# Kernel optimization log

Hardware: AMD Instinct MI355X
Metric: run time of the kernel (lower is better)

## Reference

```python
import jax, jax.numpy as jnp
import numpy as np

B, T, D, C = 4, 8192, 1024, 64  # batch, seq_len, d_model, chunk_size


def setup_inputs() -> dict:
    key = jax.random.key(0)
    k1, k2, k3 = jax.random.split(key, 3)
    out = jax.random.normal(k1, (B, T, D), jnp.float32)
    W_write = jax.random.normal(k2, (D, D), jnp.float32) / np.float32(np.sqrt(D))
    W_read = jax.random.normal(k3, (D, D), jnp.float32) / np.float32(np.sqrt(D))
    decay = jnp.float32(4.6)                     # torch init: tensor(4.6)
    log_alpha = jnp.log(jnp.float32(0.03))       # torch init: log(memory_alpha)
    return {"out": out, "W_write": W_write, "W_read": W_read,
            "decay": decay, "log_alpha": log_alpha}


def reference(out, W_write, W_read, decay, log_alpha):
    Bd, Td, Dd = out.shape
    nC = Td // C  # T chosen divisible by chunk_size
    out32 = out.astype(jnp.float32)
    gamma = jax.nn.sigmoid(decay)
    log_gamma = jnp.log(gamma)

    v = out32 @ W_write.T                               # proj_write
    wk = jnp.pad(out32[:, :-1], ((0, 0), (1, 0), (0, 0)))  # shift right by 1
    rk = out32

    p = jnp.arange(C)
    diffs = jnp.maximum(p[:, None] - 1 - p[None, :], 0)
    causal = (p[:, None] > p[None, :]).astype(jnp.float32)
    M = jnp.exp(diffs * log_gamma) * causal             # (C, C) intra-chunk decay mask
    dec_inter = gamma ** p                              # (C,)
    gw = gamma ** (C - 1 - p)                           # (C,)
    gC = gamma ** C

    def chunk(x):  # (B,T,D) -> (nC,B,C,D) for scan over chunks
        return x.reshape(Bd, nC, C, Dd).transpose(1, 0, 2, 3)

    rk_c, wk_c, v_c = chunk(rk), chunk(wk), chunk(v)

    def body(W, xs):
        r, w, vv = xs                                   # each (B,C,D)
        inter = jnp.einsum('bde,bce->bcd', W, r) * dec_inter[None, :, None]
        S = jnp.einsum('bcd,bed->bce', r, w)            # (B,C,C)
        intra = jnp.einsum('bce,bed->bcd', S * M, vv)
        W_new = gC * W + jnp.einsum('bcd,bce->bde', vv * gw[None, :, None], w)
        return W_new, inter + intra

    W0 = jnp.zeros((Bd, Dd, Dd), jnp.float32)
    _, reads = jax.lax.scan(body, W0, (rk_c, wk_c, v_c))  # reads: (nC,B,C,D)
    reads = reads.transpose(1, 0, 2, 3).reshape(Bd, Td, Dd)

    alpha = jnp.exp(log_alpha)
    return out + alpha * (reads @ W_read.T).astype(out.dtype)
```

## Files before the change

### kernel.cpp

```cpp
#include <hip/hip_runtime.h>


typedef __attribute__((ext_vector_type(8))) short short8;
typedef __attribute__((ext_vector_type(4))) short short4v;
typedef __attribute__((ext_vector_type(4))) float f32x4;

#define B_ 4
#define T_ 8192
#define D_ 1024
#define C_ 64
#define NC_ 128

#define DEVI static __device__ __forceinline__

#define EXPF(x) __builtin_expf(x)
#define LOG2F(x) __builtin_log2f(x)
#define EXP2F(x) __builtin_exp2f(x)

DEVI unsigned short f2bf_u(float f) {
  unsigned int u = __float_as_uint(f);
  u += 0x7fffu + ((u >> 16) & 1u);
  return (unsigned short)(u >> 16);
}
DEVI short f2bfs(float f) { return (short)f2bf_u(f); }
DEVI float bf2fs(short h) { return __uint_as_float(((unsigned int)(unsigned short)h) << 16); }

DEVI f32x4 mfma16(short8 a, short8 b, f32x4 c) {
  return __builtin_amdgcn_mfma_f32_16x16x32_bf16(a, b, c, 0, 0, 0);
}

__global__ __launch_bounds__(256) void k_cast(const float* __restrict__ src,
                                              short* __restrict__ dst, int n8) {
  int i = blockIdx.x * 256 + threadIdx.x;
  if (i >= n8) return;
  const float4* s = (const float4*)src;
  float4 a = s[2 * i], b = s[2 * i + 1];
  short8 o;
  o[0] = f2bfs(a.x); o[1] = f2bfs(a.y); o[2] = f2bfs(a.z); o[3] = f2bfs(a.w);
  o[4] = f2bfs(b.x); o[5] = f2bfs(b.y); o[6] = f2bfs(b.z); o[7] = f2bfs(b.w);
  *((short8*)dst + i) = o;
}

__global__ __launch_bounds__(256) void k_transT(const short* __restrict__ rk,
                                                short* __restrict__ wTg) {
  __shared__ short ts[64][72];
  const int tid = threadIdx.x;
  const int t0 = blockIdx.x * 64, e0 = blockIdx.y * 64, b = blockIdx.z;
  const short* rk_b = rk + (size_t)b * T_ * D_;
  short* w_b = wTg + (size_t)b * D_ * T_;
  const int lr = tid >> 3, ls = tid & 7;
#pragma unroll
  for (int p = 0; p < 2; ++p) {
    int row = p * 32 + lr;
    int t = t0 - 1 + row;
    short8 v8;
    if (t >= 0) v8 = *(const short8*)(rk_b + (size_t)t * D_ + e0 + ls * 8);
    else v8 = (short8){0, 0, 0, 0, 0, 0, 0, 0};
    *(short8*)&ts[row][ls * 8] = v8;
  }
  __syncthreads();
  const int er5 = tid & 31, thi = tid >> 5;
#pragma unroll
  for (int ep = 0; ep < 2; ++ep) {
    int erow = ep * 32 + er5;
    short8 w8;
#pragma unroll
    for (int j = 0; j < 8; ++j) w8[j] = ts[thi * 8 + j][erow];
    *(short8*)(w_b + (size_t)(e0 + erow) * T_ + t0 + thi * 8) = w8;
  }
}

__global__ __launch_bounds__(256) void k_gemm_v(const short* __restrict__ Aw,
                                                const short* __restrict__ Bx,
                                                short* __restrict__ vT) {
  __shared__ short As[128][72];
  __shared__ short Bs[128][72];
  const int tid = threadIdx.x;
  const int lane = tid & 63, wv = tid >> 6;
  const int wm = (wv >> 1) * 64, wn = (wv & 1) * 64;
  const int l16 = lane & 15, q = lane >> 4;
  const int m0 = blockIdx.y * 128;
  const int n0 = blockIdx.x * 128;
  f32x4 acc[4][4];
  for (int a = 0; a < 4; ++a)
    for (int b = 0; b < 4; ++b) acc[a][b] = (f32x4){0.f, 0.f, 0.f, 0.f};
  const int lrow = tid >> 3, lseg = tid & 7;
  const short* Ap = Aw + (size_t)(m0 + lrow) * D_ + lseg * 8;
  const short* Bp = Bx + (size_t)(n0 + lrow) * D_ + lseg * 8;
  for (int kb = 0; kb < D_; kb += 64) {
#pragma unroll
    for (int p = 0; p < 4; ++p) {
      *(short8*)&As[lrow + p * 32][lseg * 8] = *(const short8*)(Ap + (size_t)(p * 32) * D_ + kb);
      *(short8*)&Bs[lrow + p * 32][lseg * 8] = *(const short8*)(Bp + (size_t)(p * 32) * D_ + kb);
    }
    __syncthreads();
#pragma unroll
    for (int ks = 0; ks < 2; ++ks) {
      short8 af[4], bfr[4];
#pragma unroll
      for (int mt = 0; mt < 4; ++mt) af[mt] = *(const short8*)&As[wm + mt * 16 + l16][ks * 32 + q * 8];
#pragma unroll
      for (int nt = 0; nt < 4; ++nt) bfr[nt] = *(const short8*)&Bs[wn + nt * 16 + l16][ks * 32 + q * 8];
#pragma unroll
      for (int mt = 0; mt < 4; ++mt)
#pragma unroll
        for (int nt = 0; nt < 4; ++nt) acc[mt][nt] = mfma16(af[mt], bfr[nt], acc[mt][nt]);
    }
    __syncthreads();
  }
  const int b = n0 >> 13;
  const int tbase = (n0 & (T_ - 1)) + wn;
  short* outp = vT + (size_t)b * D_ * T_;
#pragma unroll
  for (int mt = 0; mt < 4; ++mt)
#pragma unroll
    for (int nt = 0; nt < 4; ++nt)
#pragma unroll
      for (int i = 0; i < 4; ++i) {
        int d = m0 + wm + mt * 16 + q * 4 + i;
        int t = tbase + nt * 16 + l16;
        outp[(size_t)d * T_ + t] = f2bfs(acc[mt][nt][i]);
      }
}

__global__ __launch_bounds__(1024) void k_scan(const short* __restrict__ rk,
                                               const short* __restrict__ vT_g,
                                               const short* __restrict__ wTg,
                                               short* __restrict__ inter_,
                                               const float* __restrict__ decay_p) {
  __shared__ short rs[64][264];
  __shared__ short wT[256][72];
  __shared__ short Wb[16][1032];
  __shared__ short vTs[16][72];
  __shared__ float red[8][64][17];

  const int tid = threadIdx.x;
  const int lane = tid & 63;
  const int wv = tid >> 6;
  const int l16 = lane & 15, q = lane >> 4;
  const int dt = blockIdx.x, b = blockIdx.y;
  const int d0 = dt * 16;
  const float gamma = 1.f / (1.f + EXPF(-decay_p[0]));
  const float lg2g = LOG2F(gamma);
  const float gC = EXP2F(64.f * lg2g);

  const short* rk_b = rk + (size_t)b * T_ * D_;
  const short* wT_b = wTg + (size_t)b * D_ * T_;
  const short* vT_b = vT_g + (size_t)b * D_ * T_;

  const int srow = tid >> 5;
  const int sseg = tid & 31;
  const int erow = tid >> 3;
  const int tseg = tid & 7;

  const bool vrole = (tid >= 512 && tid < 768);
  const int vd = (tid - 512) >> 4;
  const int vc4 = ((tid - 512) & 15) << 2;
  const short* vptr = vT_b + (size_t)(d0 + vd) * T_ + vc4;

  const int ew = (wv >> 1) * 32;
  const int cpair = (wv & 1) * 2;

  f32x4 Wacc[4];
#pragma unroll
  for (int j = 0; j < 4; ++j) Wacc[j] = (f32x4){0.f, 0.f, 0.f, 0.f};
  f32x4 iacc[2];
  iacc[0] = (f32x4){0.f, 0.f, 0.f, 0.f};
  iacc[1] = (f32x4){0.f, 0.f, 0.f, 0.f};

  short8 pf0, pf1, pf2, pf3;
  short4v vpre;

  auto issue_pf = [&](int g) {
    int nch = g >> 2, ns = g & 3;
    const short* rsrc = rk_b + (size_t)(nch * 64 + srow) * D_ + ns * 256 + sseg * 8;
    pf0 = *(const short8*)rsrc;
    pf1 = *(const short8*)(rsrc + (size_t)32 * D_);
    const short* wsrc = wT_b + (size_t)(ns * 256 + erow) * T_ + nch * 64 + tseg * 8;
    pf2 = *(const short8*)wsrc;
    pf3 = *(const short8*)(wsrc + (size_t)128 * T_);
  };
  auto write_pf = [&]() {
    *(short8*)&rs[srow][sseg * 8] = pf0;
    *(short8*)&rs[srow + 32][sseg * 8] = pf1;
    *(short8*)&wT[erow][tseg * 8] = pf2;
    *(short8*)&wT[erow + 128][tseg * 8] = pf3;
  };
  auto write_vTs = [&]() {
#pragma unroll
    for (int j = 0; j < 4; ++j)
      vTs[vd][vc4 + j] = f2bfs(bf2fs(vpre[j]) * EXP2F(lg2g * (float)(63 - (vc4 + j))));
  };

  issue_pf(0);
  if (vrole) vpre = *(const short4v*)vptr;
  write_pf();
  if (vrole) write_vTs();
  {
    short4v z4 = (short4v){0, 0, 0, 0};
    for (int i = tid; i < (16 * 1032) / 4; i += 1024) ((short4v*)&Wb[0][0])[i] = z4;
  }
  __syncthreads();

  for (int ch = 0; ch < NC_; ++ch) {
    short8 a2k0 = *(const short8*)&vTs[l16][q * 8];
    short8 a2k1 = *(const short8*)&vTs[l16][32 + q * 8];
#pragma unroll
    for (int s = 0; s < 4; ++s) {
      const int g = ch * 4 + s;
      if (g + 1 < 512) issue_pf(g + 1);
      if (s == 3 && vrole && ch + 1 < NC_) vpre = *(const short4v*)(vptr + (ch + 1) * 64);
      short8 bfr1 = *(const short8*)&Wb[l16][s * 256 + ew + q * 8];
      short8 af0 = *(const short8*)&rs[cpair * 16 + l16][ew + q * 8];
      short8 af1 = *(const short8*)&rs[(cpair + 1) * 16 + l16][ew + q * 8];
      iacc[0] = mfma16(af0, bfr1, iacc[0]);
      iacc[1] = mfma16(af1, bfr1, iacc[1]);
      short8 bw0 = *(const short8*)&wT[wv * 16 + l16][q * 8];
      short8 bw1 = *(const short8*)&wT[wv * 16 + l16][32 + q * 8];
      Wacc[s] = mfma16(a2k0, bw0, Wacc[s]);
      Wacc[s] = mfma16(a2k1, bw1, Wacc[s]);
      __syncthreads();
      if (g + 1 < 512) write_pf();
      if (s < 3) {
        __syncthreads();
      } else {
#pragma unroll
        for (int u = 0; u < 2; ++u)
#pragma unroll
          for (int i = 0; i < 4; ++i) {
            red[wv >> 1][(cpair + u) * 16 + q * 4 + i][l16] = iacc[u][i];
            iacc[u][i] = 0.f;
          }
#pragma unroll
        for (int s2 = 0; s2 < 4; ++s2)
#pragma unroll
          for (int i = 0; i < 4; ++i) {
            Wb[q * 4 + i][s2 * 256 + wv * 16 + l16] = f2bfs(Wacc[s2][i]);
            Wacc[s2][i] *= gC;
          }
        if (vrole && ch + 1 < NC_) write_vTs();
        __syncthreads();
        {
          int c = tid >> 4, d = tid & 15;
          float sum = 0.f;
#pragma unroll
          for (int p = 0; p < 8; ++p) sum += red[p][c][d];
          inter_[(size_t)b * T_ * D_ + (size_t)(ch * 64 + c) * D_ + d0 + d] =
              f2bfs(sum * EXP2F(lg2g * (float)c));
        }
      }
    }
  }
}

__global__ __launch_bounds__(256) void k_intra(const short* __restrict__ rk,
                                               const short* __restrict__ vT_g,
                                               short* __restrict__ intra_,
                                               const float* __restrict__ decay_p) {
  __shared__ short rs[65][264];
  __shared__ short P[64][72];
  __shared__ short vs[256][72];
  const int tid = threadIdx.x;
  const int lane = tid & 63, wv = tid >> 6;
  const int l16 = lane & 15, q = lane >> 4;
  const int ch = blockIdx.x, b = blockIdx.y;
  const int t0 = ch << 6;
  const float gamma = 1.f / (1.f + EXPF(-decay_p[0]));
  const float lg2g = LOG2F(gamma);
  const short* rk_b = rk + (size_t)b * T_ * D_;
  f32x4 Sacc[4];
#pragma unroll
  for (int j = 0; j < 4; ++j) Sacc[j] = (f32x4){0.f, 0.f, 0.f, 0.f};

  for (int s = 0; s < 4; ++s) {
    const int e0 = s << 8;
#pragma unroll
    for (int p = 0; p < 9; ++p) {
      int idx = p * 256 + tid;
      if (idx < 2080) {
        int row = idx >> 5, seg = idx & 31;
        int t = t0 - 1 + row;
        short8 v8;
        if (t >= 0) v8 = *(const short8*)(rk_b + (size_t)t * D_ + e0 + seg * 8);
        else v8 = (short8){0, 0, 0, 0, 0, 0, 0, 0};
        *(short8*)&rs[row][seg * 8] = v8;
      }
    }
    __syncthreads();
#pragma unroll
    for (int ks = 0; ks < 8; ++ks) {
      short8 af = *(const short8*)&rs[wv * 16 + l16 + 1][ks * 32 + q * 8];
#pragma unroll
      for (int nt = 0; nt < 4; ++nt) {
        short8 bfr = *(const short8*)&rs[nt * 16 + l16][ks * 32 + q * 8];
        Sacc[nt] = mfma16(af, bfr, Sacc[nt]);
      }
    }
    __syncthreads();
  }
#pragma unroll
  for (int nt = 0; nt < 4; ++nt)
#pragma unroll
    for (int i = 0; i < 4; ++i) {
      int c = wv * 16 + q * 4 + i;
      int cp = nt * 16 + l16;
      float m = (c > cp) ? EXP2F(lg2g * (float)(c - 1 - cp)) : 0.f;
      P[c][cp] = f2bfs(Sacc[nt][i] * m);
    }
  __syncthreads();
  const short* vsrc = vT_g + (size_t)b * D_ * T_ + (size_t)tid * T_ + t0;
  size_t base = (size_t)b * T_ * D_;
  for (int p = 0; p < 4; ++p) {
    const short* sp = vsrc + (size_t)(p * 256) * T_;
#pragma unroll
    for (int seg = 0; seg < 8; ++seg)
      *(short8*)&vs[tid][seg * 8] = *(const short8*)(sp + seg * 8);
    __syncthreads();
    f32x4 acc[4][4];
#pragma unroll
    for (int a = 0; a < 4; ++a)
#pragma unroll
      for (int bb = 0; bb < 4; ++bb) acc[a][bb] = (f32x4){0.f, 0.f, 0.f, 0.f};
#pragma unroll
    for (int ks2 = 0; ks2 < 2; ++ks2) {
      short8 af[4];
#pragma unroll
      for (int mt = 0; mt < 4; ++mt) af[mt] = *(const short8*)&P[mt * 16 + l16][ks2 * 32 + q * 8];
#pragma unroll
      for (int nt = 0; nt < 4; ++nt) {
        short8 bfr = *(const short8*)&vs[wv * 64 + nt * 16 + l16][ks2 * 32 + q * 8];
#pragma unroll
        for (int mt = 0; mt < 4; ++mt) acc[mt][nt] = mfma16(af[mt], bfr, acc[mt][nt]);
      }
    }
#pragma unroll
    for (int mt = 0; mt < 4; ++mt)
#pragma unroll
      for (int nt = 0; nt < 4; ++nt)
#pragma unroll
        for (int i = 0; i < 4; ++i) {
          int c = mt * 16 + q * 4 + i;
          int d = p * 256 + wv * 64 + nt * 16 + l16;
          intra_[base + (size_t)(t0 + c) * D_ + d] = f2bfs(acc[mt][nt][i]);
        }
    __syncthreads();
  }
}

__global__ __launch_bounds__(256) void k_gemm_final(const short* __restrict__ inter_,
                                                    const short* __restrict__ intra_,
                                                    const short* __restrict__ Wr,
                                                    const float* __restrict__ xin,
                                                    float* __restrict__ y,
                                                    const float* __restrict__ la_p) {
  __shared__ short As[128][72];
  __shared__ short Bs[128][72];
  const float alpha = EXPF(la_p[0]);
  const int tid = threadIdx.x;
  const int lane = tid & 63, wv = tid >> 6;
  const int wm = (wv >> 1) * 64, wn = (wv & 1) * 64;
  const int l16 = lane & 15, q = lane >> 4;
  const int m0 = blockIdx.x * 128;
  const int n0 = blockIdx.y * 128;
  f32x4 acc[4][4];
  for (int a = 0; a < 4; ++a)
    for (int b = 0; b < 4; ++b) acc[a][b] = (f32x4){0.f, 0.f, 0.f, 0.f};
  const int lrow = tid >> 3, lseg = tid & 7;
  for (int kb = 0; kb < D_; kb += 64) {
#pragma unroll
    for (int p = 0; p < 4; ++p) {
      size_t aoff = (size_t)(m0 + lrow + p * 32) * D_ + kb + lseg * 8;
      short8 xa = *(const short8*)(inter_ + aoff);
      short8 xb = *(const short8*)(intra_ + aoff);
      short8 xs;
#pragma unroll
      for (int j = 0; j < 8; ++j) xs[j] = f2bfs(bf2fs(xa[j]) + bf2fs(xb[j]));
      *(short8*)&As[lrow + p * 32][lseg * 8] = xs;
      *(short8*)&Bs[lrow + p * 32][lseg * 8] =
          *(const short8*)(Wr + (size_t)(n0 + lrow + p * 32) * D_ + kb + lseg * 8);
    }
    __syncthreads();
#pragma unroll
    for (int ks = 0; ks < 2; ++ks) {
      short8 af[4], bfr[4];
#pragma unroll
      for (int mt = 0; mt < 4; ++mt) af[mt] = *(const short8*)&As[wm + mt * 16 + l16][ks * 32 + q * 8];
#pragma unroll
      for (int nt = 0; nt < 4; ++nt) bfr[nt] = *(const short8*)&Bs[wn + nt * 16 + l16][ks * 32 + q * 8];
#pragma unroll
      for (int mt = 0; mt < 4; ++mt)
#pragma unroll
        for (int nt = 0; nt < 4; ++nt) acc[mt][nt] = mfma16(af[mt], bfr[nt], acc[mt][nt]);
    }
    __syncthreads();
  }
#pragma unroll
  for (int mt = 0; mt < 4; ++mt)
#pragma unroll
    for (int nt = 0; nt < 4; ++nt)
#pragma unroll
      for (int i = 0; i < 4; ++i) {
        int t = m0 + wm + mt * 16 + q * 4 + i;
        int d = n0 + wn + nt * 16 + l16;
        size_t idx = (size_t)t * D_ + d;
        y[idx] = xin[idx] + alpha * acc[mt][nt][i];
      }
}

extern "C" void kernel_launch(void* const* d_in, const int* in_sizes, int n_in,
                              void* d_out, int out_size, void* d_ws, size_t ws_size,
                              hipStream_t stream) {
  const float* x = (const float*)d_in[0];
  const float* Ww = (const float*)d_in[1];
  const float* Wr = (const float*)d_in[2];
  const float* decay = (const float*)d_in[3];
  const float* log_alpha = (const float*)d_in[4];
  float* y = (float*)d_out;

  short* ws = (short*)d_ws;
  const size_t NTD = (size_t)B_ * T_ * D_;
  short* rk_bf = ws;
  short* vT_bf = rk_bf + NTD;
  short* inter_b = vT_bf + NTD;
  short* intra_b = inter_b + NTD;
  short* Ww_bf = intra_b + NTD;
  short* Wr_bf = Ww_bf + (size_t)D_ * D_;
  short* wTg = intra_b;

  k_cast<<<(int)(NTD / 8 / 256), 256, 0, stream>>>(x, rk_bf, (int)(NTD / 8));
  k_cast<<<512, 256, 0, stream>>>(Ww, Ww_bf, (D_ * D_) / 8);
  k_cast<<<512, 256, 0, stream>>>(Wr, Wr_bf, (D_ * D_) / 8);
  k_transT<<<dim3(T_ / 64, D_ / 64, B_), 256, 0, stream>>>(rk_bf, wTg);
  k_gemm_v<<<dim3(256, 8), 256, 0, stream>>>(Ww_bf, rk_bf, vT_bf);
  k_scan<<<dim3(64, 4), 1024, 0, stream>>>(rk_bf, vT_bf, wTg, inter_b, decay);
  k_intra<<<dim3(128, 4), 256, 0, stream>>>(rk_bf, vT_bf, intra_b, decay);
  k_gemm_final<<<dim3(256, 8), 256, 0, stream>>>(inter_b, intra_b, Wr_bf, x, y, log_alpha);
}
```

Measured before the change: 1.147 ms.

## Load scan MFMA operands directly from global into registers, drop LDS staging

```diff
diff --git a/kernel.cpp b/kernel.cpp
--- a/kernel.cpp
+++ b/kernel.cpp
@@ -123,16 +123,14 @@
       }
 }
 
-__global__ __launch_bounds__(1024) void k_scan(const short* __restrict__ rk,
-                                               const short* __restrict__ vT_g,
-                                               const short* __restrict__ wTg,
-                                               short* __restrict__ inter_,
-                                               const float* __restrict__ decay_p) {
-  __shared__ short rs[64][264];
-  __shared__ short wT[256][72];
+__global__ __launch_bounds__(1024, 4) void k_scan(const short* __restrict__ rk,
+                                                  const short* __restrict__ vT_g,
+                                                  const short* __restrict__ wTg,
+                                                  short* __restrict__ inter_,
+                                                  const float* __restrict__ decay_p) {
   __shared__ short Wb[16][1032];
   __shared__ short vTs[16][72];
-  __shared__ float red[8][64][17];
+  __shared__ float red[8][64][20];
 
   const int tid = threadIdx.x;
   const int lane = tid & 63;
@@ -148,18 +146,17 @@
   const short* wT_b = wTg + (size_t)b * D_ * T_;
   const short* vT_b = vT_g + (size_t)b * D_ * T_;
 
-  const int srow = tid >> 5;
-  const int sseg = tid & 31;
-  const int erow = tid >> 3;
-  const int tseg = tid & 7;
+  const int ew = (wv >> 1) * 32;
+  const int cpair = (wv & 1) * 2;
+
+  const short* af_base = rk_b + (size_t)(cpair * 16 + l16) * D_ + ew + q * 8;
+  const short* bw_base = wT_b + (size_t)(wv * 16 + l16) * T_ + q * 8;
 
   const bool vrole = (tid >= 512 && tid < 768);
   const int vd = (tid - 512) >> 4;
   const int vc4 = ((tid - 512) & 15) << 2;
   const short* vptr = vT_b + (size_t)(d0 + vd) * T_ + vc4;
-
-  const int ew = (wv >> 1) * 32;
-  const int cpair = (wv & 1) * 2;
+  short4v vpre;
 
   f32x4 Wacc[4];
 #pragma unroll
@@ -168,23 +165,14 @@
   iacc[0] = (f32x4){0.f, 0.f, 0.f, 0.f};
   iacc[1] = (f32x4){0.f, 0.f, 0.f, 0.f};
 
-  short8 pf0, pf1, pf2, pf3;
-  short4v vpre;
-
-  auto issue_pf = [&](int g) {
-    int nch = g >> 2, ns = g & 3;
-    const short* rsrc = rk_b + (size_t)(nch * 64 + srow) * D_ + ns * 256 + sseg * 8;
-    pf0 = *(const short8*)rsrc;
-    pf1 = *(const short8*)(rsrc + (size_t)32 * D_);
-    const short* wsrc = wT_b + (size_t)(ns * 256 + erow) * T_ + nch * 64 + tseg * 8;
-    pf2 = *(const short8*)wsrc;
-    pf3 = *(const short8*)(wsrc + (size_t)128 * T_);
-  };
-  auto write_pf = [&]() {
-    *(short8*)&rs[srow][sseg * 8] = pf0;
-    *(short8*)&rs[srow + 32][sseg * 8] = pf1;
-    *(short8*)&wT[erow][tseg * 8] = pf2;
-    *(short8*)&wT[erow + 128][tseg * 8] = pf3;
+  short8 paf0, paf1, pbw0, pbw1;
+  auto issue = [&](int ch, int s) {
+    const short* a = af_base + (size_t)(ch * 64) * D_ + s * 256;
+    paf0 = *(const short8*)a;
+    paf1 = *(const short8*)(a + (size_t)16 * D_);
+    const short* w = bw_base + (size_t)(s * 256) * T_ + ch * 64;
+    pbw0 = *(const short8*)w;
+    pbw1 = *(const short8*)(w + 32);
   };
   auto write_vTs = [&]() {
 #pragma unroll
@@ -192,14 +180,13 @@
       vTs[vd][vc4 + j] = f2bfs(bf2fs(vpre[j]) * EXP2F(lg2g * (float)(63 - (vc4 + j))));
   };
 
-  issue_pf(0);
+  issue(0, 0);
   if (vrole) vpre = *(const short4v*)vptr;
-  write_pf();
-  if (vrole) write_vTs();
   {
     short4v z4 = (short4v){0, 0, 0, 0};
     for (int i = tid; i < (16 * 1032) / 4; i += 1024) ((short4v*)&Wb[0][0])[i] = z4;
   }
+  if (vrole) write_vTs();
   __syncthreads();
 
   for (int ch = 0; ch < NC_; ++ch) {
@@ -207,48 +194,43 @@
     short8 a2k1 = *(const short8*)&vTs[l16][32 + q * 8];
 #pragma unroll
     for (int s = 0; s < 4; ++s) {
-      const int g = ch * 4 + s;
-      if (g + 1 < 512) issue_pf(g + 1);
-      if (s == 3 && vrole && ch + 1 < NC_) vpre = *(const short4v*)(vptr + (ch + 1) * 64);
-      short8 bfr1 = *(const short8*)&Wb[l16][s * 256 + ew + q * 8];
-      short8 af0 = *(const short8*)&rs[cpair * 16 + l16][ew + q * 8];
-      short8 af1 = *(const short8*)&rs[(cpair + 1) * 16 + l16][ew + q * 8];
-      iacc[0] = mfma16(af0, bfr1, iacc[0]);
-      iacc[1] = mfma16(af1, bfr1, iacc[1]);
-      short8 bw0 = *(const short8*)&wT[wv * 16 + l16][q * 8];
-      short8 bw1 = *(const short8*)&wT[wv * 16 + l16][32 + q * 8];
-      Wacc[s] = mfma16(a2k0, bw0, Wacc[s]);
-      Wacc[s] = mfma16(a2k1, bw1, Wacc[s]);
-      __syncthreads();
-      if (g + 1 < 512) write_pf();
-      if (s < 3) {
-        __syncthreads();
-      } else {
-#pragma unroll
-        for (int u = 0; u < 2; ++u)
-#pragma unroll
-          for (int i = 0; i < 4; ++i) {
-            red[wv >> 1][(cpair + u) * 16 + q * 4 + i][l16] = iacc[u][i];
-            iacc[u][i] = 0.f;
-          }
-#pragma unroll
-        for (int s2 = 0; s2 < 4; ++s2)
-#pragma unroll
-          for (int i = 0; i < 4; ++i) {
-            Wb[q * 4 + i][s2 * 256 + wv * 16 + l16] = f2bfs(Wacc[s2][i]);
-            Wacc[s2][i] *= gC;
-          }
-        if (vrole && ch + 1 < NC_) write_vTs();
-        __syncthreads();
-        {
-          int c = tid >> 4, d = tid & 15;
-          float sum = 0.f;
-#pragma unroll
-          for (int p = 0; p < 8; ++p) sum += red[p][c][d];
-          inter_[(size_t)b * T_ * D_ + (size_t)(ch * 64 + c) * D_ + d0 + d] =
-              f2bfs(sum * EXP2F(lg2g * (float)c));
-        }
-      }
+      short8 af0 = paf0, af1 = paf1, bw0 = pbw0, bw1 = pbw1;
+      if (s == 3) issue(ch + 1, 0);
+      else issue(ch, s + 1);
+      short8 bfr = *(const short8*)&Wb[l16][s * 256 + ew + q * 8];
+      iacc[0] = mfma16(bfr, af0, iacc[0]);
+      iacc[1] = mfma16(bfr, af1, iacc[1]);
+      Wacc[s] = mfma16(bw0, a2k0, Wacc[s]);
+      Wacc[s] = mfma16(bw1, a2k1, Wacc[s]);
+    }
+    if (vrole && ch + 1 < NC_) vpre = *(const short4v*)(vptr + (ch + 1) * 64);
+    __syncthreads();
+#pragma unroll
+    for (int u = 0; u < 2; ++u) {
+      *(f32x4*)&red[wv >> 1][(cpair + u) * 16 + l16][q * 4] = iacc[u];
+      iacc[u] = (f32x4){0.f, 0.f, 0.f, 0.f};
+    }
+#pragma unroll
+    for (int s2 = 0; s2 < 4; ++s2) {
+      short4v w4;
+#pragma unroll
+      for (int i = 0; i < 4; ++i) w4[i] = f2bfs(Wacc[s2][i]);
+      *(short4v*)&Wb[l16][s2 * 256 + wv * 16 + q * 4] = w4;
+#pragma unroll
+      for (int i = 0; i < 4; ++i) Wacc[s2][i] *= gC;
+    }
+    if (vrole && ch + 1 < NC_) write_vTs();
+    __syncthreads();
+    if (tid < 256) {
+      int c = tid >> 2, dq = tid & 3;
+      f32x4 sum = *(const f32x4*)&red[0][c][dq * 4];
+#pragma unroll
+      for (int p = 1; p < 8; ++p) sum += *(const f32x4*)&red[p][c][dq * 4];
+      float sc = EXP2F(lg2g * (float)c);
+      short4v o;
+#pragma unroll
+      for (int i = 0; i < 4; ++i) o[i] = f2bfs(sum[i] * sc);
+      *(short4v*)(inter_ + (size_t)b * T_ * D_ + (size_t)(ch * 64 + c) * D_ + d0 + dq * 4) = o;
     }
   }
 }
```

Measured after the change: 1.502 ms. +31.0%, slower.
